# Optimization experiments

Hardware: AMD Instinct MI355X
Metric: run time of the kernel (lower is better)

Reference implementation:

```python
import jax, jax.numpy as jnp
import numpy as np

N, C, E, K = 50000, 128, 640000, 40  # nodes, feat dim, edges, classes
EPS = 1e-5


def setup_inputs() -> dict:
    key = jax.random.key(0)
    ks = jax.random.split(key, 8)
    s = 1.0 / np.sqrt(C)
    return {
        "x": jax.random.normal(ks[0], (N, C), jnp.float32),
        "edge_index": jax.random.randint(ks[1], (2, E), 0, N, dtype=jnp.int32),
        "W_conv": jax.random.normal(ks[2], (C, C), jnp.float32) * s,
        "b_conv": jnp.zeros((C,), jnp.float32),
        "gamma": jnp.ones((C,), jnp.float32),
        "beta": jnp.zeros((C,), jnp.float32),
        "W_fc": jax.random.normal(ks[3], (C, K), jnp.float32) * s,
        "b_fc": jnp.zeros((K,), jnp.float32),
    }


def reference(x, edge_index, W_conv, b_conv, gamma, beta, W_fc, b_fc):
    n = x.shape[0]
    loops = jnp.arange(n, dtype=edge_index.dtype)
    src = jnp.concatenate([edge_index[0], loops])  # add self-loops (PyG default)
    dst = jnp.concatenate([edge_index[1], loops])
    # symmetric normalization: deg^{-1/2}[src] * deg^{-1/2}[dst]
    deg = jax.ops.segment_sum(jnp.ones_like(dst, jnp.float32), dst, num_segments=n)
    dinv = jax.lax.rsqrt(jnp.maximum(deg, 1.0))  # deg >= 1 with self-loops
    norm = dinv[src] * dinv[dst]  # [E+N]
    h = x @ W_conv  # [N, C] transform before propagate (GCNConv)
    agg = jax.ops.segment_sum(h[src] * norm[:, None], dst, num_segments=n) + b_conv
    a = jax.nn.relu(agg) * x  # dropout = identity (eval mode); elementwise mul with residual
    mu = jnp.mean(a, axis=-1, keepdims=True)
    var = jnp.mean((a - mu) ** 2, axis=-1, keepdims=True)
    ln = (a - mu) * jax.lax.rsqrt(var + EPS) * gamma + beta
    return (ln + x) @ W_fc + b_fc
```

## Files before the change

### kernel.cpp

```cpp
#include <hip/hip_runtime.h>

#define C_DIM 128
#define EPS 1e-5f
#define CSTRIDE 16

typedef __attribute__((ext_vector_type(8))) short short8;
typedef __attribute__((ext_vector_type(4))) float f32x4;

__device__ __forceinline__ unsigned bf16rn(float f) {
    unsigned u = __float_as_uint(f);
    return (u + 0x7fffu + ((u >> 16) & 1u)) >> 16;
}
__device__ __forceinline__ unsigned pack_bf16(float lo, float hi) {
    return bf16rn(lo) | (bf16rn(hi) << 16);
}
__device__ __forceinline__ float blo(unsigned u) { return __uint_as_float(u << 16); }
__device__ __forceinline__ float bhi(unsigned u) { return __uint_as_float(u & 0xffff0000u); }

__global__ void prep0(const float* __restrict__ W, const float* __restrict__ Wfc,
                      unsigned short* __restrict__ WhT, unsigned short* __restrict__ WlT,
                      unsigned short* __restrict__ WT,
                      float4* __restrict__ cz, int czn) {
    int gid = blockIdx.x * blockDim.x + threadIdx.x;
    int stride = gridDim.x * blockDim.x;
    for (int t = gid; t < 128 * 128; t += stride) {
        int c = t >> 7, k = t & 127;
        float v = W[k * 128 + c];
        unsigned hi = bf16rn(v);
        float fh = __uint_as_float(hi << 16);
        WhT[c * 128 + k] = (unsigned short)hi;
        WlT[c * 128 + k] = (unsigned short)bf16rn(v - fh);
    }
    for (int t = gid; t < 48 * 128; t += stride) {
        int nc = t >> 7, k = t & 127;
        WT[nc * 128 + k] = (unsigned short)((nc < 40) ? bf16rn(Wfc[k * 40 + nc]) : 0u);
    }
    float4 z = make_float4(0.f, 0.f, 0.f, 0.f);
    for (int t = gid; t < czn; t += stride) cz[t] = z;
}

__global__ __launch_bounds__(256, 4) void fat(const float* __restrict__ x,
                                              const unsigned short* __restrict__ WhT,
                                              const unsigned short* __restrict__ WlT,
                                              unsigned short* __restrict__ hbs,
                                              const int* __restrict__ esrc,
                                              const int* __restrict__ edst,
                                              int* __restrict__ cntA,
                                              int* __restrict__ cntB,
                                              unsigned short* __restrict__ bsrcu,
                                              int n, int e, int g1) {
    int b = blockIdx.x;
    int t = threadIdx.x;

    if (b < g1) {
        int r0 = b * 128;
        int wid = t >> 6, lane = t & 63;
        int mrow = lane & 15, quad = lane >> 4;
        int rb = r0 + wid * 32;

        f32x4 acc[2][8];
#pragma unroll
        for (int m = 0; m < 2; m++)
#pragma unroll
            for (int nn = 0; nn < 8; nn++) acc[m][nn] = (f32x4){0.f, 0.f, 0.f, 0.f};

#pragma unroll
        for (int ks = 0; ks < 4; ks++) {
            short8 Ah[2], Al[2];
#pragma unroll
            for (int m = 0; m < 2; m++) {
                int r = rb + m * 16 + mrow;
                if (r >= n) r = n - 1;
                const float* xp = &x[(long)r * C_DIM + ks * 32 + quad * 8];
                float4 va = *(const float4*)xp;
                float4 vb = *(const float4*)(xp + 4);
                float xv[8] = {va.x, va.y, va.z, va.w, vb.x, vb.y, vb.z, vb.w};
#pragma unroll
                for (int e8 = 0; e8 < 8; e8++) {
                    unsigned hi = bf16rn(xv[e8]);
                    Ah[m][e8] = (short)hi;
                    Al[m][e8] = (short)bf16rn(xv[e8] - __uint_as_float(hi << 16));
                }
            }
#pragma unroll
            for (int nn = 0; nn < 8; nn++) {
                int wof = (nn * 16 + mrow) * 128 + ks * 32 + quad * 8;
                short8 Bh = *(const short8*)&WhT[wof];
                short8 Bl = *(const short8*)&WlT[wof];
#pragma unroll
                for (int m = 0; m < 2; m++) {
                    acc[m][nn] = __builtin_amdgcn_mfma_f32_16x16x32_bf16(Ah[m], Bh, acc[m][nn], 0, 0, 0);
                    acc[m][nn] = __builtin_amdgcn_mfma_f32_16x16x32_bf16(Al[m], Bh, acc[m][nn], 0, 0, 0);
                    acc[m][nn] = __builtin_amdgcn_mfma_f32_16x16x32_bf16(Ah[m], Bl, acc[m][nn], 0, 0, 0);
                }
            }
        }
#pragma unroll
        for (int m = 0; m < 2; m++)
#pragma unroll
            for (int nn = 0; nn < 8; nn++) {
                int c = nn * 16 + mrow;
#pragma unroll
                for (int reg = 0; reg < 4; reg++) {
                    int r = rb + m * 16 + quad * 4 + reg;
                    if (r < n) hbs[(long)r * 128 + c] = (unsigned short)bf16rn(acc[m][nn][reg]);
                }
            }
    } else {
        int sb = b - g1;
        int q = (e + 3) >> 2;
        int i0 = sb * 256 + t;
        int i1 = i0 + q, i2 = i0 + 2 * q, i3 = i0 + 3 * q;
        bool v0 = i0 < e, v1 = i1 < e, v2 = i2 < e, v3 = i3 < e;
        int d0 = v0 ? edst[i0] : 0, s0 = v0 ? esrc[i0] : 0;
        int d1 = v1 ? edst[i1] : 0, s1 = v1 ? esrc[i1] : 0;
        int d2 = v2 ? edst[i2] : 0, s2 = v2 ? esrc[i2] : 0;
        int d3 = v3 ? edst[i3] : 0, s3 = v3 ? esrc[i3] : 0;
        int p0 = v0 ? atomicAdd(&cntA[(long)d0 * CSTRIDE], 1) : 64;
        int p1 = v1 ? atomicAdd(&cntA[(long)d1 * CSTRIDE], 1) : 64;
        int p2 = v2 ? atomicAdd(&cntB[(long)d2 * CSTRIDE], 1) : 64;
        int p3 = v3 ? atomicAdd(&cntB[(long)d3 * CSTRIDE], 1) : 64;
        if (p0 < 64) bsrcu[(long)d0 * 64 + p0] = (unsigned short)s0;
        if (p1 < 64) bsrcu[(long)d1 * 64 + p1] = (unsigned short)s1;
        if (p2 < 64) bsrcu[(long)d2 * 64 + 63 - p2] = (unsigned short)s2;
        if (p3 < 64) bsrcu[(long)d3 * 64 + 63 - p3] = (unsigned short)s3;
    }
}

__global__ __launch_bounds__(256) void aggregate(const unsigned* __restrict__ hb,
                                                 const float* __restrict__ x,
                                                 const int* __restrict__ cntA,
                                                 const int* __restrict__ cntB,
                                                 const unsigned short* __restrict__ bsrcu,
                                                 const float* __restrict__ bconv,
                                                 const float* __restrict__ gamma,
                                                 const float* __restrict__ beta,
                                                 unsigned* __restrict__ zb, int n) {
    int wid = (blockIdx.x * blockDim.x + threadIdx.x) >> 6;
    if (wid >= n) return;
    int lane = threadIdx.x & 63;
    int sub = lane & 15, grp = lane >> 4;
    int i = wid;

    uint4 us = *(const uint4*)(hb + (long)i * 64 + sub * 4);
    float4 xa = *(const float4*)&x[(long)i * C_DIM + sub * 8];
    float4 xb = *(const float4*)&x[(long)i * C_DIM + sub * 8 + 4];

    int dA = cntA[(long)i * CSTRIDE], dB = cntB[(long)i * CSTRIDE];
    float di = rsqrtf((float)(dA + dB) + 1.0f);
    if (dA > 64) dA = 64;
    if (dB > 64 - dA) dB = 64 - dA;
    int tot = dA + dB;
    int shift = 64 - tot;

    int sraw = (int)bsrcu[(long)i * 64 + lane];
    bool valid = (lane < dA) | (lane >= 64 - dB);
    int s_all = valid ? sraw : 0;
    float w_all = 0.f;
    if (valid)
        w_all = rsqrtf((float)(cntA[(long)s_all * CSTRIDE] + cntB[(long)s_all * CSTRIDE]) + 1.0f) * di;

    float wself = (grp == 0) ? di * di : 0.f;
    float acc[8];
    acc[0] = wself * blo(us.x); acc[1] = wself * bhi(us.x);
    acc[2] = wself * blo(us.y); acc[3] = wself * bhi(us.y);
    acc[4] = wself * blo(us.z); acc[5] = wself * bhi(us.z);
    acc[6] = wself * blo(us.w); acc[7] = wself * bhi(us.w);

    int nIt = (tot + 15) >> 4;
    for (int it = 0; it < nIt; ++it) {
        int tb = grp + it * 16;
        int ss[4];
        float ww[4];
#pragma unroll
        for (int qq = 0; qq < 4; qq++) {
            int tq = tb + qq * 4;
            int slq = ((tq < dA) ? tq : tq + shift) & 63;
            int sq = __shfl(s_all, slq);
            float wq = __shfl(w_all, slq);
            if (tq >= tot) { wq = 0.f; sq = i; }
            ss[qq] = sq;
            ww[qq] = wq;
        }
        uint4 u[4];
#pragma unroll
        for (int qq = 0; qq < 4; qq++) u[qq] = *(const uint4*)(hb + (long)ss[qq] * 64 + sub * 4);
#pragma unroll
        for (int qq = 0; qq < 4; qq++) {
            float w = ww[qq];
            acc[0] += w * blo(u[qq].x); acc[1] += w * bhi(u[qq].x);
            acc[2] += w * blo(u[qq].y); acc[3] += w * bhi(u[qq].y);
            acc[4] += w * blo(u[qq].z); acc[5] += w * bhi(u[qq].z);
            acc[6] += w * blo(u[qq].w); acc[7] += w * bhi(u[qq].w);
        }
    }

#pragma unroll
    for (int j = 0; j < 8; j++) {
        acc[j] += __shfl_xor(acc[j], 16);
        acc[j] += __shfl_xor(acc[j], 32);
    }

    float4 bca = *(const float4*)&bconv[sub * 8];
    float4 bcb = *(const float4*)&bconv[sub * 8 + 4];
    float a[8], xv[8];
    xv[0] = xa.x; xv[1] = xa.y; xv[2] = xa.z; xv[3] = xa.w;
    xv[4] = xb.x; xv[5] = xb.y; xv[6] = xb.z; xv[7] = xb.w;
    float bc[8] = {bca.x, bca.y, bca.z, bca.w, bcb.x, bcb.y, bcb.z, bcb.w};
#pragma unroll
    for (int j = 0; j < 8; j++) a[j] = fmaxf(acc[j] + bc[j], 0.f) * xv[j];

    float s = a[0] + a[1] + a[2] + a[3] + a[4] + a[5] + a[6] + a[7];
#pragma unroll
    for (int off = 1; off < 16; off <<= 1) s += __shfl_xor(s, off);
    float mu = s * (1.0f / 128.0f);
    float d[8], v = 0.f;
#pragma unroll
    for (int j = 0; j < 8; j++) { d[j] = a[j] - mu; v += d[j] * d[j]; }
#pragma unroll
    for (int off = 1; off < 16; off <<= 1) v += __shfl_xor(v, off);
    float inv = rsqrtf(v * (1.0f / 128.0f) + EPS);

    if (grp == 0) {
        float4 ga = *(const float4*)&gamma[sub * 8];
        float4 gb = *(const float4*)&gamma[sub * 8 + 4];
        float4 ba = *(const float4*)&beta[sub * 8];
        float4 bb = *(const float4*)&beta[sub * 8 + 4];
        float g[8] = {ga.x, ga.y, ga.z, ga.w, gb.x, gb.y, gb.z, gb.w};
        float be[8] = {ba.x, ba.y, ba.z, ba.w, bb.x, bb.y, bb.z, bb.w};
        float o[8];
#pragma unroll
        for (int j = 0; j < 8; j++) o[j] = d[j] * inv * g[j] + be[j] + xv[j];
        uint4 p;
        p.x = pack_bf16(o[0], o[1]);
        p.y = pack_bf16(o[2], o[3]);
        p.z = pack_bf16(o[4], o[5]);
        p.w = pack_bf16(o[6], o[7]);
        *(uint4*)(zb + (long)i * 64 + sub * 4) = p;
    }
}

__global__ __launch_bounds__(256) void gemm2(const unsigned short* __restrict__ zb,
                                             const unsigned short* __restrict__ WT,
                                             const float* __restrict__ bfc,
                                             float* __restrict__ out, int n) {
    int t = threadIdx.x;
    int w = t >> 6, lane = t & 63;
    int r0 = (blockIdx.x * 4 + w) * 64;
    if (r0 >= n) return;
    int mrow = lane & 15;
    int quad = lane >> 4;
    f32x4 acc[4][3];
#pragma unroll
    for (int m = 0; m < 4; m++)
#pragma unroll
        for (int nt = 0; nt < 3; nt++) acc[m][nt] = (f32x4){0.f, 0.f, 0.f, 0.f};
#pragma unroll
    for (int ks = 0; ks < 4; ks++) {
        short8 A[4], B[3];
#pragma unroll
        for (int m = 0; m < 4; m++) {
            int r = r0 + m * 16 + mrow;
            if (r >= n) r = n - 1;
            A[m] = *(const short8*)&zb[(long)r * 128 + ks * 32 + quad * 8];
        }
#pragma unroll
        for (int nt = 0; nt < 3; nt++)
            B[nt] = *(const short8*)&WT[(nt * 16 + mrow) * 128 + ks * 32 + quad * 8];
#pragma unroll
        for (int m = 0; m < 4; m++)
#pragma unroll
            for (int nt = 0; nt < 3; nt++)
                acc[m][nt] = __builtin_amdgcn_mfma_f32_16x16x32_bf16(A[m], B[nt], acc[m][nt], 0, 0, 0);
    }
#pragma unroll
    for (int nt = 0; nt < 3; nt++) {
        int c = nt * 16 + mrow;
        if (c < 40) {
            float bias = bfc[c];
#pragma unroll
            for (int m = 0; m < 4; m++) {
#pragma unroll
                for (int reg = 0; reg < 4; reg++) {
                    int r = r0 + m * 16 + quad * 4 + reg;
                    if (r < n) out[(long)r * 40 + c] = acc[m][nt][reg] + bias;
                }
            }
        }
    }
}

extern "C" void kernel_launch(void* const* d_in, const int* in_sizes, int n_in,
                              void* d_out, int out_size, void* d_ws, size_t ws_size,
                              hipStream_t stream) {
    const float* x     = (const float*)d_in[0];
    const int*   ei    = (const int*)d_in[1];
    const float* Wc    = (const float*)d_in[2];
    const float* bc    = (const float*)d_in[3];
    const float* gamma = (const float*)d_in[4];
    const float* beta  = (const float*)d_in[5];
    const float* Wfc   = (const float*)d_in[6];
    const float* bfc   = (const float*)d_in[7];
    float* out = (float*)d_out;

    int N = in_sizes[0] / C_DIM;
    int E = in_sizes[1] / 2;
    const int* esrc = ei;
    const int* edst = ei + E;

    char* p = (char*)d_ws;
    auto carve = [&](size_t bytes) {
        void* q = (void*)p;
        p += (bytes + 255) & ~(size_t)255;
        return q;
    };
    unsigned* hb        = (unsigned*)carve((size_t)N * 64 * 4);
    unsigned* zb        = (unsigned*)carve((size_t)N * 64 * 4);
    unsigned short* WT  = (unsigned short*)carve(48 * 128 * 2);
    unsigned short* WhT = (unsigned short*)carve(128 * 128 * 2);
    unsigned short* WlT = (unsigned short*)carve(128 * 128 * 2);
    int* cntA           = (int*)carve((size_t)N * CSTRIDE * 4);
    int* cntB           = (int*)carve((size_t)N * CSTRIDE * 4);
    unsigned short* bsrcu = (unsigned short*)carve((size_t)N * 64 * 2);

    int czn = (N * CSTRIDE * 2) / 4;
    prep0<<<256, 256, 0, stream>>>(Wc, Wfc, WhT, WlT, WT, (float4*)cntA, czn);

    int g1 = (N + 127) / 128;
    int nscat = (((E + 3) >> 2) + 255) / 256;
    fat<<<g1 + nscat, 256, 0, stream>>>(x, WhT, WlT, (unsigned short*)hb, esrc, edst,
                                        cntA, cntB, bsrcu, N, E, g1);

    aggregate<<<((size_t)N * 64 + 255) / 256, 256, 0, stream>>>(
        hb, x, cntA, cntB, bsrcu, bc, gamma, beta, zb, N);

    gemm2<<<(N / 64 + 4) / 4, 256, 0, stream>>>((const unsigned short*)zb, WT, bfc, out, N);
}
```

Baseline: 196.5 us.

## Pre-scale features by source degree factor in a separate pass, shrink gemm2 tiles

```diff
diff --git a/kernel.cpp b/kernel.cpp
--- a/kernel.cpp
+++ b/kernel.cpp
@@ -127,7 +127,24 @@
     }
 }
 
-__global__ __launch_bounds__(256) void aggregate(const unsigned* __restrict__ hb,
+__global__ __launch_bounds__(256) void d0(const unsigned* __restrict__ hb,
+                                          const int* __restrict__ cntA,
+                                          const int* __restrict__ cntB,
+                                          unsigned* __restrict__ hb2, int n) {
+    int gid = blockIdx.x * 256 + threadIdx.x;
+    if (gid >= n * 16) return;
+    int row = gid >> 4;
+    float di = rsqrtf((float)(cntA[(long)row * CSTRIDE] + cntB[(long)row * CSTRIDE]) + 1.0f);
+    uint4 u = ((const uint4*)hb)[gid];
+    uint4 o;
+    o.x = pack_bf16(di * blo(u.x), di * bhi(u.x));
+    o.y = pack_bf16(di * blo(u.y), di * bhi(u.y));
+    o.z = pack_bf16(di * blo(u.z), di * bhi(u.z));
+    o.w = pack_bf16(di * blo(u.w), di * bhi(u.w));
+    ((uint4*)hb2)[gid] = o;
+}
+
+__global__ __launch_bounds__(256) void aggregate(const unsigned* __restrict__ hb2,
                                                  const float* __restrict__ x,
                                                  const int* __restrict__ cntA,
                                                  const int* __restrict__ cntB,
@@ -142,9 +159,10 @@
     int sub = lane & 15, grp = lane >> 4;
     int i = wid;
 
-    uint4 us = *(const uint4*)(hb + (long)i * 64 + sub * 4);
+    uint4 us = *(const uint4*)(hb2 + (long)i * 64 + sub * 4);
     float4 xa = *(const float4*)&x[(long)i * C_DIM + sub * 8];
     float4 xb = *(const float4*)&x[(long)i * C_DIM + sub * 8 + 4];
+    int sraw = (int)bsrcu[(long)i * 64 + lane];
 
     int dA = cntA[(long)i * CSTRIDE], dB = cntB[(long)i * CSTRIDE];
     float di = rsqrtf((float)(dA + dB) + 1.0f);
@@ -153,14 +171,9 @@
     int tot = dA + dB;
     int shift = 64 - tot;
 
-    int sraw = (int)bsrcu[(long)i * 64 + lane];
-    bool valid = (lane < dA) | (lane >= 64 - dB);
-    int s_all = valid ? sraw : 0;
-    float w_all = 0.f;
-    if (valid)
-        w_all = rsqrtf((float)(cntA[(long)s_all * CSTRIDE] + cntB[(long)s_all * CSTRIDE]) + 1.0f) * di;
-
-    float wself = (grp == 0) ? di * di : 0.f;
+    int s_all = ((lane < dA) | (lane >= 64 - dB)) ? sraw : 0;
+
+    float wself = (grp == 0) ? 1.f : 0.f;
     float acc[8];
     acc[0] = wself * blo(us.x); acc[1] = wself * bhi(us.x);
     acc[2] = wself * blo(us.y); acc[3] = wself * bhi(us.y);
@@ -177,14 +190,14 @@
             int tq = tb + qq * 4;
             int slq = ((tq < dA) ? tq : tq + shift) & 63;
             int sq = __shfl(s_all, slq);
-            float wq = __shfl(w_all, slq);
+            float wq = 1.f;
             if (tq >= tot) { wq = 0.f; sq = i; }
             ss[qq] = sq;
             ww[qq] = wq;
         }
         uint4 u[4];
 #pragma unroll
-        for (int qq = 0; qq < 4; qq++) u[qq] = *(const uint4*)(hb + (long)ss[qq] * 64 + sub * 4);
+        for (int qq = 0; qq < 4; qq++) u[qq] = *(const uint4*)(hb2 + (long)ss[qq] * 64 + sub * 4);
 #pragma unroll
         for (int qq = 0; qq < 4; qq++) {
             float w = ww[qq];
@@ -208,7 +221,7 @@
     xv[4] = xb.x; xv[5] = xb.y; xv[6] = xb.z; xv[7] = xb.w;
     float bc[8] = {bca.x, bca.y, bca.z, bca.w, bcb.x, bcb.y, bcb.z, bcb.w};
 #pragma unroll
-    for (int j = 0; j < 8; j++) a[j] = fmaxf(acc[j] + bc[j], 0.f) * xv[j];
+    for (int j = 0; j < 8; j++) a[j] = fmaxf(acc[j] * di + bc[j], 0.f) * xv[j];
 
     float s = a[0] + a[1] + a[2] + a[3] + a[4] + a[5] + a[6] + a[7];
 #pragma unroll
@@ -246,32 +259,25 @@
                                              float* __restrict__ out, int n) {
     int t = threadIdx.x;
     int w = t >> 6, lane = t & 63;
-    int r0 = (blockIdx.x * 4 + w) * 64;
+    int r0 = blockIdx.x * 64 + w * 16;
     if (r0 >= n) return;
     int mrow = lane & 15;
     int quad = lane >> 4;
-    f32x4 acc[4][3];
-#pragma unroll
-    for (int m = 0; m < 4; m++)
-#pragma unroll
-        for (int nt = 0; nt < 3; nt++) acc[m][nt] = (f32x4){0.f, 0.f, 0.f, 0.f};
+    f32x4 acc[3];
+#pragma unroll
+    for (int nt = 0; nt < 3; nt++) acc[nt] = (f32x4){0.f, 0.f, 0.f, 0.f};
 #pragma unroll
     for (int ks = 0; ks < 4; ks++) {
-        short8 A[4], B[3];
-#pragma unroll
-        for (int m = 0; m < 4; m++) {
-            int r = r0 + m * 16 + mrow;
-            if (r >= n) r = n - 1;
-            A[m] = *(const short8*)&zb[(long)r * 128 + ks * 32 + quad * 8];
-        }
+        int r = r0 + mrow;
+        if (r >= n) r = n - 1;
+        short8 A = *(const short8*)&zb[(long)r * 128 + ks * 32 + quad * 8];
+        short8 B[3];
 #pragma unroll
         for (int nt = 0; nt < 3; nt++)
             B[nt] = *(const short8*)&WT[(nt * 16 + mrow) * 128 + ks * 32 + quad * 8];
 #pragma unroll
-        for (int m = 0; m < 4; m++)
-#pragma unroll
-            for (int nt = 0; nt < 3; nt++)
-                acc[m][nt] = __builtin_amdgcn_mfma_f32_16x16x32_bf16(A[m], B[nt], acc[m][nt], 0, 0, 0);
+        for (int nt = 0; nt < 3; nt++)
+            acc[nt] = __builtin_amdgcn_mfma_f32_16x16x32_bf16(A, B[nt], acc[nt], 0, 0, 0);
     }
 #pragma unroll
     for (int nt = 0; nt < 3; nt++) {
@@ -279,12 +285,9 @@
         if (c < 40) {
             float bias = bfc[c];
 #pragma unroll
-            for (int m = 0; m < 4; m++) {
-#pragma unroll
-                for (int reg = 0; reg < 4; reg++) {
-                    int r = r0 + m * 16 + quad * 4 + reg;
-                    if (r < n) out[(long)r * 40 + c] = acc[m][nt][reg] + bias;
-                }
+            for (int reg = 0; reg < 4; reg++) {
+                int r = r0 + quad * 4 + reg;
+                if (r < n) out[(long)r * 40 + c] = acc[nt][reg] + bias;
             }
         }
     }
@@ -315,7 +318,7 @@
         return q;
     };
     unsigned* hb        = (unsigned*)carve((size_t)N * 64 * 4);
-    unsigned* zb        = (unsigned*)carve((size_t)N * 64 * 4);
+    unsigned* hb2       = (unsigned*)carve((size_t)N * 64 * 4);
     unsigned short* WT  = (unsigned short*)carve(48 * 128 * 2);
     unsigned short* WhT = (unsigned short*)carve(128 * 128 * 2);
     unsigned short* WlT = (unsigned short*)carve(128 * 128 * 2);
@@ -323,6 +326,8 @@
     int* cntB           = (int*)carve((size_t)N * CSTRIDE * 4);
     unsigned short* bsrcu = (unsigned short*)carve((size_t)N * 64 * 2);
 
+    unsigned* zb = hb;
+
     int czn = (N * CSTRIDE * 2) / 4;
     prep0<<<256, 256, 0, stream>>>(Wc, Wfc, WhT, WlT, WT, (float4*)cntA, czn);
 
@@ -331,8 +336,10 @@
     fat<<<g1 + nscat, 256, 0, stream>>>(x, WhT, WlT, (unsigned short*)hb, esrc, edst,
                                         cntA, cntB, bsrcu, N, E, g1);
 
+    d0<<<(N * 16 + 255) / 256, 256, 0, stream>>>(hb, cntA, cntB, hb2, N);
+
     aggregate<<<((size_t)N * 64 + 255) / 256, 256, 0, stream>>>(
-        hb, x, cntA, cntB, bsrcu, bc, gamma, beta, zb, N);
-
-    gemm2<<<(N / 64 + 4) / 4, 256, 0, stream>>>((const unsigned short*)zb, WT, bfc, out, N);
-}
+        hb2, x, cntA, cntB, bsrcu, bc, gamma, beta, zb, N);
+
+    gemm2<<<(N + 63) / 64, 256, 0, stream>>>((const unsigned short*)zb, WT, bfc, out, N);
+}
```

New measurement: 185.0 us. 5.9% less time.
